# Performance work log

Measured on AMD Instinct MI355X. Metric: run time of the kernel, lower is better.

The kernel has to match this reference:

```python
import jax, jax.numpy as jnp
import numpy as np

LOW_RANK = 8   # q passed to torch.svd_lowrank
NITER = 2      # torch.svd_lowrank default power-iteration count


def setup_inputs() -> dict:
    key = jax.random.key(0)
    k1, k2 = jax.random.split(key)
    x = jax.random.normal(k1, (32, 256, 56, 56), dtype=jnp.float32)
    # Gaussian test matrix used by torch.svd_lowrank's range finder on A^T:
    # R = randn(A.mT.shape[-1]=C, q), shared across the (H*W) batch.
    omega = jax.random.normal(k2, (256, LOW_RANK), dtype=jnp.float32)
    return {"x": x, "omega": omega}


def _qr_q(a):
    # reduced QR, batched over leading dims; inputs are tall (m >= n)
    return jnp.linalg.qr(a, mode="reduced")[0]


def reference(x, omega):
    B, C, H, W = x.shape
    # [B,C,H,W] -> [H,W,C,B] -> (H*W, C, B): H*W small matrices A of shape (C, B)
    A = jnp.transpose(x, (2, 3, 1, 0)).reshape(H * W, C, B)

    # torch.svd_lowrank with n=B > q takes the transposed branch:
    #   Q = get_approximate_basis(A^T, q, niter=2)   (Q: (B, q), orthonormal cols)
    #   U S V^T == (A @ Q) @ Q^T  -> reconstruction is A Q Q^T
    Y = jnp.einsum("mcb,cq->mbq", A, omega)      # A^T @ Omega : (M, B, q)
    Q = _qr_q(Y)
    for _ in range(NITER):
        Z = jnp.einsum("mcb,mbq->mcq", A, Q)     # A @ Q       : (M, C, q)
        Qc = _qr_q(Z)
        Y = jnp.einsum("mcb,mcq->mbq", A, Qc)    # A^T @ Qc    : (M, B, q)
        Q = _qr_q(Y)

    P = jnp.einsum("mcb,mbq->mcq", A, Q)         # A @ Q       : (M, C, q)
    y = jnp.einsum("mcq,mbq->mcb", P, Q)         # A Q Q^T     : (M, C, B)

    y = y.reshape(H, W, C, B)
    return jnp.transpose(y, (3, 2, 0, 1))        # back to [B, C, H, W]
```

## Files before the change

kernel.cpp:

```cpp
#include <hip/hip_runtime.h>
#include <math.h>

#define HW   3136
#define NB   32
#define NC   256
#define TM   16
#define CC   8
#define LDP  36
#define SLABC (TM * LDP)
#define SLABF (CC * SLABC)

#define NS   4
#define CSL  (NC / NS)
#define NCH  (CSL / CC)
#define GK   1280
#define PST  68

#define YT_(mi,b,q) Sm[(mi)*265 + (q)*33 + (b)]
#define WT_(mi,b,q) Sm[4240 + (mi)*265 + (q)*33 + (b)]
#define SS_(mi,k)   Sm[8480 + (mi)*65 + (k)]
#define SMEMF 9520

__host__ __device__ constexpr int TRI(int i, int j) { return i*8 - (i*(i+1))/2 + j; }

__device__ __forceinline__ void stage_load512(float4* r, const float* __restrict__ xg,
                                              int c0, int m0, int t) {
#pragma unroll
  for (int i = 0; i < 2; ++i) {
    int id = t + i * 512;
    int cc = id >> 7, b = (id >> 2) & 31, mq = id & 3;
    r[i] = *reinterpret_cast<const float4*>(
        xg + (size_t)(b * NC + c0 + cc) * HW + m0 + mq * 4);
  }
}
__device__ __forceinline__ void stage_write_t(const float4* r, float* sl, int t) {
#pragma unroll
  for (int i = 0; i < 2; ++i) {
    int id = t + i * 512;
    int cc = id >> 7, b = (id >> 2) & 31, mq = id & 3;
    float* p = sl + cc * SLABC + (mq * 4) * LDP + b;
    p[0 * LDP] = r[i].x;
    p[1 * LDP] = r[i].y;
    p[2 * LDP] = r[i].z;
    p[3 * LDP] = r[i].w;
  }
}

__device__ __forceinline__ void chol8(const float* __restrict__ Sm, int mi, float* Rl) {
#pragma unroll
  for (int i = 0; i < 8; ++i) {
    float d = SS_(mi, i * 8 + i);
#pragma unroll
    for (int k = 0; k < 8; ++k) {
      if (k < i) { float rk = Rl[TRI(k, i)]; d = fmaf(-rk, rk, d); }
    }
    float rii = sqrtf(fmaxf(d, 1e-30f));
    float inv = 1.0f / rii;
    Rl[TRI(i, i)] = inv;
#pragma unroll
    for (int j = 0; j < 8; ++j) {
      if (j > i) {
        float v = SS_(mi, i * 8 + j);
#pragma unroll
        for (int k = 0; k < 8; ++k) {
          if (k < i) v = fmaf(-Rl[TRI(k, i)], Rl[TRI(k, j)], v);
        }
        Rl[TRI(i, j)] = v * inv;
      }
    }
  }
}

__device__ __forceinline__ void trsm1row(const float* __restrict__ srcB, float* __restrict__ dstB,
                                         int mi, int r, const float* Rl) {
  float yv[8], qv[8];
#pragma unroll
  for (int q = 0; q < 8; ++q) yv[q] = srcB[mi * 265 + q * 33 + r];
#pragma unroll
  for (int j = 0; j < 8; ++j) {
    float a = yv[j];
#pragma unroll
    for (int k = 0; k < 8; ++k) {
      if (k < j) a = fmaf(-qv[k], Rl[TRI(k, j)], a);
    }
    qv[j] = a * Rl[TRI(j, j)];
  }
#pragma unroll
  for (int q = 0; q < 8; ++q) dstB[mi * 265 + q * 33 + r] = qv[q];
}

__device__ __forceinline__ void cholqr32(float* __restrict__ Sm, int mi, int r) {
#pragma unroll
  for (int e = 0; e < 2; ++e) {
    int idx = r + e * 32, i = idx >> 3, j = idx & 7;
    float s = 0.f;
#pragma unroll
    for (int b = 0; b < 32; ++b) s = fmaf(YT_(mi, b, i), YT_(mi, b, j), s);
    SS_(mi, idx) = s;
  }
  __syncthreads();
  float Rl[36];
  chol8(Sm, mi, Rl);
  trsm1row(Sm, Sm, mi, r, Rl);
  __syncthreads();
}

__global__ __launch_bounds__(512, 4) void tsvd_k1a(const float* __restrict__ x,
                                                   const float* __restrict__ omega,
                                                   float* __restrict__ Gp) {
  __shared__ float Sm[2 * SLABF];
  const int t = threadIdx.x;
  const int mi = t & 15, g = t >> 4;
  const int rg = g >> 3, bj = g & 7;
  const int r0 = rg * 8, b0 = bj * 4;
  const int s = blockIdx.x & (NS - 1);
  const int mt = blockIdx.x / NS;
  const int m0 = mt * TM, m = m0 + mi;
  const int c0 = s * CSL;

  float Gt[8][4], Yt[8];
#pragma unroll
  for (int i = 0; i < 8; ++i) {
    Yt[i] = 0.f;
#pragma unroll
    for (int j = 0; j < 4; ++j) Gt[i][j] = 0.f;
  }

  float4 st[2];
  stage_load512(st, x, c0, m0, t);
  stage_write_t(st, Sm, t);
  for (int ch = 0; ch < NCH; ++ch) {
    if (ch + 1 < NCH) stage_load512(st, x, c0 + (ch + 1) * CC, m0, t);
    __syncthreads();
    const float* cur = Sm + (ch & 1) * SLABF;
#pragma unroll
    for (int cc = 0; cc < CC; ++cc) {
      const int c = c0 + ch * CC + cc;
      const float* v = cur + cc * SLABC + mi * LDP;
      float4 ra = *reinterpret_cast<const float4*>(v + r0);
      float4 rb = *reinterpret_cast<const float4*>(v + r0 + 4);
      float4 cb = *reinterpret_cast<const float4*>(v + b0);
      const float w = omega[c * 8 + bj];
      float rv[8] = {ra.x, ra.y, ra.z, ra.w, rb.x, rb.y, rb.z, rb.w};
#pragma unroll
      for (int i = 0; i < 8; ++i) {
        Gt[i][0] = fmaf(rv[i], cb.x, Gt[i][0]);
        Gt[i][1] = fmaf(rv[i], cb.y, Gt[i][1]);
        Gt[i][2] = fmaf(rv[i], cb.z, Gt[i][2]);
        Gt[i][3] = fmaf(rv[i], cb.w, Gt[i][3]);
        Yt[i]    = fmaf(rv[i], w,    Yt[i]);
      }
    }
    if (ch + 1 < NCH) stage_write_t(st, Sm + ((ch + 1) & 1) * SLABF, t);
  }

  float4* rec = reinterpret_cast<float4*>(Gp + ((size_t)s * HW + m) * GK);
#pragma unroll
  for (int i = 0; i < 8; ++i)
    rec[(r0 + i) * 8 + bj] = make_float4(Gt[i][0], Gt[i][1], Gt[i][2], Gt[i][3]);
  float* recf = Gp + ((size_t)s * HW + m) * GK + 1024;
#pragma unroll
  for (int i = 0; i < 8; ++i)
    recf[(r0 + i) * 8 + bj] = Yt[i];
}

__global__ __launch_bounds__(256) void tsvd_k1b(const float* __restrict__ Gp,
                                                float* __restrict__ Qws) {
  __shared__ float Sm[SMEMF];
  const int t = threadIdx.x;
  const int r = t & 31, mi = t >> 5;
  const int m0 = blockIdx.x * 8, m = m0 + mi;

  float G0[32], Y0[8];
#pragma unroll
  for (int b = 0; b < 32; ++b) G0[b] = 0.f;
#pragma unroll
  for (int q = 0; q < 8; ++q) Y0[q] = 0.f;
#pragma unroll
  for (int s = 0; s < NS; ++s) {
    const float4* rec = reinterpret_cast<const float4*>(Gp + ((size_t)s * HW + m) * GK);
#pragma unroll
    for (int k = 0; k < 8; ++k) {
      float4 v = rec[r * 8 + k];
      G0[4 * k + 0] += v.x;
      G0[4 * k + 1] += v.y;
      G0[4 * k + 2] += v.z;
      G0[4 * k + 3] += v.w;
    }
    float4 y0 = rec[256 + r * 2 + 0];
    float4 y1 = rec[256 + r * 2 + 1];
    Y0[0] += y0.x; Y0[1] += y0.y; Y0[2] += y0.z; Y0[3] += y0.w;
    Y0[4] += y1.x; Y0[5] += y1.y; Y0[6] += y1.z; Y0[7] += y1.w;
  }

#pragma unroll
  for (int q = 0; q < 8; ++q) YT_(mi, r, q) = Y0[q];
  __syncthreads();

#pragma unroll
  for (int it = 0; it < 3; ++it) {
    cholqr32(Sm, mi, r);
    cholqr32(Sm, mi, r);
    if (it < 2) {
      float u[8];
#pragma unroll
      for (int q = 0; q < 8; ++q) {
        float a = 0.f;
#pragma unroll
        for (int b = 0; b < 32; ++b) a = fmaf(G0[b], YT_(mi, b, q), a);
        u[q] = a;
      }
#pragma unroll
      for (int q = 0; q < 8; ++q) WT_(mi, r, q) = u[q];
      __syncthreads();
#pragma unroll
      for (int e = 0; e < 2; ++e) {
        int idx = r + e * 32, i2 = idx >> 3, j2 = idx & 7;
        float a = 0.f;
#pragma unroll
        for (int b = 0; b < 32; ++b) a = fmaf(YT_(mi, b, i2), WT_(mi, b, j2), a);
        SS_(mi, idx) = a;
      }
      __syncthreads();
      {
        float Rl[36];
        chol8(Sm, mi, Rl);
        trsm1row(Sm, Sm + 4240, mi, r, Rl);
      }
      __syncthreads();
#pragma unroll
      for (int q = 0; q < 8; ++q) {
        float a = 0.f;
#pragma unroll
        for (int b = 0; b < 32; ++b) a = fmaf(G0[b], WT_(mi, b, q), a);
        u[q] = a;
      }
#pragma unroll
      for (int q = 0; q < 8; ++q) YT_(mi, r, q) = u[q];
      __syncthreads();
    }
  }

  float q0[8];
#pragma unroll
  for (int q = 0; q < 8; ++q) q0[q] = YT_(mi, r, q);
  float4* qrec = reinterpret_cast<float4*>(Qws + (size_t)m * 256);
  qrec[r * 2 + 0] = make_float4(q0[0], q0[1], q0[2], q0[3]);
  qrec[r * 2 + 1] = make_float4(q0[4], q0[5], q0[6], q0[7]);
}

__global__ __launch_bounds__(512, 4) void tsvd_k2(const float* __restrict__ x,
                                                  const float* __restrict__ Qws,
                                                  float* __restrict__ y) {
  __shared__ float Sm2[2 * SLABF + TM * PST];
  float* Pl = Sm2 + 2 * SLABF;
  const int t = threadIdx.x;
  const int mi = t & 15, g = t >> 4;
  const int cj = g & 7, qd = g >> 3;
  const int r = g;
  const int bid = blockIdx.x;
  const int mt = bid % 196, cq = bid / 196;
  const int m0 = mt * TM, m = m0 + mi;
  const int cbase = cq * 32;

  const float* qrec = Qws + (size_t)m * 256;
  float Qc0[32], Qc1[32];
#pragma unroll
  for (int b = 0; b < 32; ++b) {
    float2 v = reinterpret_cast<const float2*>(qrec)[b * 4 + qd];
    Qc0[b] = v.x; Qc1[b] = v.y;
  }
  float Qr[8];
  {
    float4 a = reinterpret_cast<const float4*>(qrec)[r * 2 + 0];
    float4 b4 = reinterpret_cast<const float4*>(qrec)[r * 2 + 1];
    Qr[0] = a.x; Qr[1] = a.y; Qr[2] = a.z; Qr[3] = a.w;
    Qr[4] = b4.x; Qr[5] = b4.y; Qr[6] = b4.z; Qr[7] = b4.w;
  }

  float4 st[2];
  stage_load512(st, x, cbase, m0, t);
  stage_write_t(st, Sm2, t);
  for (int ch = 0; ch < 4; ++ch) {
    if (ch + 1 < 4) stage_load512(st, x, cbase + (ch + 1) * CC, m0, t);
    __syncthreads();
    const float* cur = Sm2 + (ch & 1) * SLABF;
    {
      const float* v = cur + cj * SLABC + mi * LDP;
      float p0 = 0.f, p1 = 0.f;
#pragma unroll
      for (int k = 0; k < 8; ++k) {
        float4 xb = *reinterpret_cast<const float4*>(v + 4 * k);
        p0 = fmaf(xb.x, Qc0[4 * k + 0], p0);
        p0 = fmaf(xb.y, Qc0[4 * k + 1], p0);
        p0 = fmaf(xb.z, Qc0[4 * k + 2], p0);
        p0 = fmaf(xb.w, Qc0[4 * k + 3], p0);
        p1 = fmaf(xb.x, Qc1[4 * k + 0], p1);
        p1 = fmaf(xb.y, Qc1[4 * k + 1], p1);
        p1 = fmaf(xb.z, Qc1[4 * k + 2], p1);
        p1 = fmaf(xb.w, Qc1[4 * k + 3], p1);
      }
      *reinterpret_cast<float2*>(Pl + mi * PST + cj * 8 + 2 * qd) = make_float2(p0, p1);
    }
    if (ch + 1 < 4) stage_write_t(st, Sm2 + ((ch + 1) & 1) * SLABF, t);
    __syncthreads();
    const float* Pm = Pl + mi * PST;
#pragma unroll
    for (int c2 = 0; c2 < 8; ++c2) {
      float4 pa = *reinterpret_cast<const float4*>(Pm + c2 * 8);
      float4 pb = *reinterpret_cast<const float4*>(Pm + c2 * 8 + 4);
      float a = 0.f;
      a = fmaf(Qr[0], pa.x, a);
      a = fmaf(Qr[1], pa.y, a);
      a = fmaf(Qr[2], pa.z, a);
      a = fmaf(Qr[3], pa.w, a);
      a = fmaf(Qr[4], pb.x, a);
      a = fmaf(Qr[5], pb.y, a);
      a = fmaf(Qr[6], pb.z, a);
      a = fmaf(Qr[7], pb.w, a);
      const int c = cbase + ch * CC + c2;
      y[((size_t)r * NC + c) * HW + m] = a;
    }
  }
}

extern "C" void kernel_launch(void* const* d_in, const int* in_sizes, int n_in,
                              void* d_out, int out_size, void* d_ws, size_t ws_size,
                              hipStream_t stream) {
  const float* x     = (const float*)d_in[0];
  const float* omega = (const float*)d_in[1];
  float* y   = (float*)d_out;
  float* Qws = (float*)d_ws;
  float* Gp  = (float*)d_out;

  tsvd_k1a<<<196 * NS, 512, 0, stream>>>(x, omega, Gp);
  tsvd_k1b<<<HW / 8, 256, 0, stream>>>(Gp, Qws);
  tsvd_k2<<<196 * 8, 512, 0, stream>>>(x, Qws, y);
}
```

Baseline: 307.9 us.

## Fuse partial Gram kernel with QR reduction via last-block atomic counter

Merges the split-C Gram/projection kernel with the follow-up reduction and power-iteration kernel. An atomic counter per 16-row tile lets the last of the four slice blocks sum the partial records and run the Cholesky-QR stage with its 512 threads. This removes a separate kernel launch and its boundary, at the cost of a memset launch, thread fences, larger shared memory per block and a serialized tail on the finishing blocks.

Measured after the change: 735.4 us. 139% more time.

```diff
diff --git a/kernel.cpp b/kernel.cpp
--- a/kernel.cpp
+++ b/kernel.cpp
@@ -105,10 +105,13 @@
   __syncthreads();
 }
 
-__global__ __launch_bounds__(512, 4) void tsvd_k1a(const float* __restrict__ x,
-                                                   const float* __restrict__ omega,
-                                                   float* __restrict__ Gp) {
-  __shared__ float Sm[2 * SLABF];
+__global__ __launch_bounds__(512, 4) void tsvd_k1(const float* __restrict__ x,
+                                                  const float* __restrict__ omega,
+                                                  float* __restrict__ Gp,
+                                                  float* __restrict__ Qws,
+                                                  int* __restrict__ cnt) {
+  __shared__ float Sm[SMEMF];
+  __shared__ int isLast;
   const int t = threadIdx.x;
   const int mi = t & 15, g = t >> 4;
   const int rg = g >> 3, bj = g & 7;
@@ -154,31 +157,33 @@
     if (ch + 1 < NCH) stage_write_t(st, Sm + ((ch + 1) & 1) * SLABF, t);
   }
 
-  float4* rec = reinterpret_cast<float4*>(Gp + ((size_t)s * HW + m) * GK);
-#pragma unroll
-  for (int i = 0; i < 8; ++i)
-    rec[(r0 + i) * 8 + bj] = make_float4(Gt[i][0], Gt[i][1], Gt[i][2], Gt[i][3]);
-  float* recf = Gp + ((size_t)s * HW + m) * GK + 1024;
-#pragma unroll
-  for (int i = 0; i < 8; ++i)
-    recf[(r0 + i) * 8 + bj] = Yt[i];
-}
-
-__global__ __launch_bounds__(256) void tsvd_k1b(const float* __restrict__ Gp,
-                                                float* __restrict__ Qws) {
-  __shared__ float Sm[SMEMF];
-  const int t = threadIdx.x;
-  const int r = t & 31, mi = t >> 5;
-  const int m0 = blockIdx.x * 8, m = m0 + mi;
-
+  {
+    float4* rec = reinterpret_cast<float4*>(Gp + ((size_t)s * HW + m) * GK);
+#pragma unroll
+    for (int i = 0; i < 8; ++i)
+      rec[(r0 + i) * 8 + bj] = make_float4(Gt[i][0], Gt[i][1], Gt[i][2], Gt[i][3]);
+    float* recf = Gp + ((size_t)s * HW + m) * GK + 1024;
+#pragma unroll
+    for (int i = 0; i < 8; ++i)
+      recf[(r0 + i) * 8 + bj] = Yt[i];
+  }
+
+  __threadfence();
+  __syncthreads();
+  if (t == 0) isLast = (atomicAdd(&cnt[mt], 1) == NS - 1) ? 1 : 0;
+  __syncthreads();
+  if (!isLast) return;
+  __threadfence();
+
+  const int r = g;
   float G0[32], Y0[8];
 #pragma unroll
   for (int b = 0; b < 32; ++b) G0[b] = 0.f;
 #pragma unroll
   for (int q = 0; q < 8; ++q) Y0[q] = 0.f;
 #pragma unroll
-  for (int s = 0; s < NS; ++s) {
-    const float4* rec = reinterpret_cast<const float4*>(Gp + ((size_t)s * HW + m) * GK);
+  for (int s2 = 0; s2 < NS; ++s2) {
+    const float4* rec = reinterpret_cast<const float4*>(Gp + ((size_t)s2 * HW + m) * GK);
 #pragma unroll
     for (int k = 0; k < 8; ++k) {
       float4 v = rec[r * 8 + k];
@@ -331,9 +336,10 @@
   const float* omega = (const float*)d_in[1];
   float* y   = (float*)d_out;
   float* Qws = (float*)d_ws;
+  int*   cnt = (int*)((char*)d_ws + (4u << 20));
   float* Gp  = (float*)d_out;
 
-  tsvd_k1a<<<196 * NS, 512, 0, stream>>>(x, omega, Gp);
-  tsvd_k1b<<<HW / 8, 256, 0, stream>>>(Gp, Qws);
+  hipMemsetAsync(cnt, 0, 196 * sizeof(int), stream);
+  tsvd_k1<<<196 * NS, 512, 0, stream>>>(x, omega, Gp, Qws, cnt);
   tsvd_k2<<<196 * 8, 512, 0, stream>>>(x, Qws, y);
 }
```
